# Performance work log

Measured on AMD Instinct MI355X. Metric: run time of the kernel, lower is better.

## Reference

```python
import jax, jax.numpy as jnp
import numpy as np

B, S, D = 2, 2048, 1024
H, HD = 16, 64


def setup_inputs() -> dict:
    key = jax.random.key(0)
    ks = jax.random.split(key, 10)
    scale = 1.0 / np.sqrt(D)
    inputs_q = jax.random.normal(ks[0], (B, S, D), dtype=jnp.float32)
    inputs_kv = jax.random.normal(ks[1], (B, S, D), dtype=jnp.float32)
    # causal mask, broadcast over batch: True = attend
    mask = jnp.broadcast_to(jnp.tril(jnp.ones((S, S), dtype=bool)), (B, S, S))
    Wq = jax.random.normal(ks[2], (D, H * HD), dtype=jnp.float32) * scale
    bq = jnp.zeros((H * HD,), dtype=jnp.float32)
    Wk = jax.random.normal(ks[3], (D, H * HD), dtype=jnp.float32) * scale
    bk = jnp.zeros((H * HD,), dtype=jnp.float32)
    Wv = jax.random.normal(ks[4], (D, H * HD), dtype=jnp.float32) * scale
    bv = jnp.zeros((H * HD,), dtype=jnp.float32)
    Wo = jax.random.normal(ks[5], (H * HD, D), dtype=jnp.float32) * scale
    bo = jnp.zeros((D,), dtype=jnp.float32)
    return {"inputs_q": inputs_q, "inputs_kv": inputs_kv, "mask": mask,
            "Wq": Wq, "bq": bq, "Wk": Wk, "bk": bk, "Wv": Wv, "bv": bv,
            "Wo": Wo, "bo": bo}


def reference(inputs_q, inputs_kv, mask, Wq, bq, Wk, bk, Wv, bv, Wo, bo):
    b, s_q, _ = inputs_q.shape
    s_k = inputs_kv.shape[1]
    # projections -> [B, S, H, HD]
    q = (inputs_q @ Wq + bq).reshape(b, s_q, H, HD)
    k = (inputs_kv @ Wk + bk).reshape(b, s_k, H, HD)
    v = (inputs_kv @ Wv + bv).reshape(b, s_k, H, HD)
    q = q / jnp.sqrt(jnp.asarray(HD, dtype=q.dtype))
    # scores: [B, H, Sq, Sk]
    attn = jnp.einsum('bqhd,bkhd->bhqk', q, k)
    m = mask[:, None, :, :]  # [B,1,Sq,Sk] broadcast over heads
    attn = jnp.where(m, attn, jnp.asarray(-1e30, dtype=attn.dtype))
    attn = jax.nn.softmax(attn, axis=-1)
    # dropout_rate = 0.0, deterministic -> identity
    out = jnp.einsum('bhqk,bkhd->bqhd', attn, v).reshape(b, s_q, H * HD)
    return out @ Wo + bo
```

## Files before the change

kernel.cpp:

```cpp
#include <hip/hip_runtime.h>

typedef __attribute__((ext_vector_type(4))) float f32x4;
typedef __attribute__((ext_vector_type(8))) short bf16x8;
typedef unsigned short u16;
typedef unsigned int u32;

#define AS1 __attribute__((address_space(1)))
#define AS3 __attribute__((address_space(3)))

__device__ __forceinline__ float fast_exp2(float x){
  return __builtin_amdgcn_exp2f(x);
}

__device__ __forceinline__ u16 f2bf(float x){
  u32 u = __float_as_uint(x);
  u += 0x7fffu + ((u >> 16) & 1u);
  return (u16)(u >> 16);
}
__device__ __forceinline__ u16 f2bf_fast(float x){
  return (u16)((__float_as_uint(x) + 0x8000u) >> 16);
}

__global__ __launch_bounds__(256) void cvt_qkv(const float* __restrict__ s0,
                                               const float* __restrict__ s1,
                                               u16* __restrict__ d0,
                                               u16* __restrict__ d1, int n4)
{
  int i = blockIdx.x * 256 + threadIdx.x;
  if (i >= n4) return;
  const float* src = blockIdx.y ? s1 : s0;
  u16* dst = blockIdx.y ? d1 : d0;
  float4 v = reinterpret_cast<const float4*>(src)[i];
  ushort4 o;
  o.x = f2bf(v.x); o.y = f2bf(v.y); o.z = f2bf(v.z); o.w = f2bf(v.w);
  reinterpret_cast<ushort4*>(dst)[i] = o;
}

__global__ __launch_bounds__(256) void transpose_cvt4(const float* __restrict__ W0,
                                                      const float* __restrict__ W1,
                                                      const float* __restrict__ W2,
                                                      const float* __restrict__ W3,
                                                      u16* __restrict__ dst)
{
  __shared__ float tile[32][33];
  const int z = blockIdx.z;
  const float* src = z == 0 ? W0 : z == 1 ? W1 : z == 2 ? W2 : W3;
  u16* d = dst + (size_t)z * 1024 * 1024;
  int tx = threadIdx.x & 31, ty = threadIdx.x >> 5;
  int k0 = blockIdx.x * 32, n0 = blockIdx.y * 32;
  for (int r = 0; r < 4; ++r)
    tile[ty + r * 8][tx] = src[(size_t)(k0 + ty + r * 8) * 1024 + n0 + tx];
  __syncthreads();
  for (int r = 0; r < 4; ++r)
    d[(size_t)(n0 + ty + r * 8) * 1024 + k0 + tx] = f2bf(tile[tx][ty + r * 8]);
}

__global__ __launch_bounds__(256) void gemm_qkv(const u16* __restrict__ Xq,
                                                const u16* __restrict__ Xkv,
                                                const u16* __restrict__ Wt,
                                                const float* __restrict__ bq,
                                                const float* __restrict__ bk,
                                                const float* __restrict__ bv,
                                                u16* __restrict__ Qb,
                                                u16* __restrict__ Kb,
                                                u16* __restrict__ Vt,
                                                int M, int K)
{
  __shared__ u16 lA[128 * 32];
  __shared__ u16 lB[128 * 32];
  const int tid = threadIdx.x;
  const int l = tid & 63, w = tid >> 6;
  const int wr = w >> 1, wc = w & 1;
  const int bm0 = blockIdx.x * 128, bn0 = blockIdx.y * 128;
  const int seg = bn0 >> 10;
  const int nloc0 = bn0 & 1023;
  const u16* A = seg ? Xkv : Xq;
  const float* bias = seg == 0 ? bq : seg == 1 ? bk : bv;
  const float scale = seg == 0 ? 0.125f * 1.44269504089f : 1.0f;
  const int lr = l & 15, lg = (l >> 4) * 8;

  f32x4 acc[4][4];
#pragma unroll
  for (int m = 0; m < 4; ++m)
#pragma unroll
    for (int n = 0; n < 4; ++n) acc[m][n] = (f32x4){0.f, 0.f, 0.f, 0.f};

  for (int k0 = 0; k0 < K; k0 += 32){
#pragma unroll
    for (int c = 0; c < 2; ++c){
      int e = (c * 256 + tid) * 8;
      int row = e >> 5, col = e & 31;
      __builtin_amdgcn_global_load_lds(
          (const AS1 u32*)(A + (size_t)(bm0 + row) * K + k0 + col),
          (AS3 u32*)(&lA[e]), 16, 0, 0);
      __builtin_amdgcn_global_load_lds(
          (const AS1 u32*)(Wt + (size_t)(bn0 + row) * K + k0 + col),
          (AS3 u32*)(&lB[e]), 16, 0, 0);
    }
    __syncthreads();
    bf16x8 aF[4], bF[4];
#pragma unroll
    for (int m = 0; m < 4; ++m)
      aF[m] = *reinterpret_cast<const bf16x8*>(&lA[(wr * 64 + m * 16 + lr) * 32 + lg]);
#pragma unroll
    for (int n = 0; n < 4; ++n)
      bF[n] = *reinterpret_cast<const bf16x8*>(&lB[(wc * 64 + n * 16 + lr) * 32 + lg]);
    __builtin_amdgcn_s_setprio(1);
#pragma unroll
    for (int m = 0; m < 4; ++m)
#pragma unroll
      for (int n = 0; n < 4; ++n)
        acc[m][n] = __builtin_amdgcn_mfma_f32_16x16x32_bf16(aF[m], bF[n], acc[m][n], 0, 0, 0);
    __builtin_amdgcn_s_setprio(0);
    __syncthreads();
  }

  const int r0 = (l >> 4) * 4;
  if (seg < 2){
    u16* C = seg == 0 ? Qb : Kb;
#pragma unroll
    for (int m = 0; m < 4; ++m)
#pragma unroll
      for (int n = 0; n < 4; ++n){
        int col = nloc0 + wc * 64 + n * 16 + lr;
        float bv_ = bias[col];
#pragma unroll
        for (int r = 0; r < 4; ++r){
          int row = bm0 + wr * 64 + m * 16 + r0 + r;
          C[(size_t)row * 1024 + col] = f2bf((acc[m][n][r] + bv_) * scale);
        }
      }
  } else {
#pragma unroll
    for (int m = 0; m < 4; ++m)
#pragma unroll
      for (int n = 0; n < 4; ++n){
        int col = nloc0 + wc * 64 + n * 16 + lr;
        float bv_ = bias[col];
        int h = col >> 6, hdl = col & 63;
#pragma unroll
        for (int r = 0; r < 4; ++r){
          int row = bm0 + wr * 64 + m * 16 + r0 + r;
          int b = row >> 11, kv = row & 2047;
          size_t off = ((size_t)(b * 16 + h)) * 131072 + (size_t)hdl * 2048 + kv;
          Vt[off] = f2bf(acc[m][n][r] + bv_);
        }
      }
  }
}

__global__ __launch_bounds__(256) void gemm_out(const u16* __restrict__ A,
                                                const u16* __restrict__ Bt,
                                                const float* __restrict__ bias,
                                                float* __restrict__ Cf,
                                                int M, int N, int K)
{
  __shared__ u16 lA[64 * 32];
  __shared__ u16 lB[128 * 32];
  const int tid = threadIdx.x;
  const int l = tid & 63, w = tid >> 6;
  const int wr = w >> 1, wc = w & 1;
  const int bm0 = blockIdx.x * 64, bn0 = blockIdx.y * 128;
  const int lr = l & 15, lg = (l >> 4) * 8;

  f32x4 acc[2][4];
#pragma unroll
  for (int m = 0; m < 2; ++m)
#pragma unroll
    for (int n = 0; n < 4; ++n) acc[m][n] = (f32x4){0.f, 0.f, 0.f, 0.f};

  for (int k0 = 0; k0 < K; k0 += 32){
    {
      int e = tid * 8;
      int row = e >> 5, col = e & 31;
      __builtin_amdgcn_global_load_lds(
          (const AS1 u32*)(A + (size_t)(bm0 + row) * K + k0 + col),
          (AS3 u32*)(&lA[e]), 16, 0, 0);
    }
#pragma unroll
    for (int c = 0; c < 2; ++c){
      int e = (c * 256 + tid) * 8;
      int row = e >> 5, col = e & 31;
      __builtin_amdgcn_global_load_lds(
          (const AS1 u32*)(Bt + (size_t)(bn0 + row) * K + k0 + col),
          (AS3 u32*)(&lB[e]), 16, 0, 0);
    }
    __syncthreads();
    bf16x8 aF[2], bF[4];
#pragma unroll
    for (int m = 0; m < 2; ++m)
      aF[m] = *reinterpret_cast<const bf16x8*>(&lA[(wr * 32 + m * 16 + lr) * 32 + lg]);
#pragma unroll
    for (int n = 0; n < 4; ++n)
      bF[n] = *reinterpret_cast<const bf16x8*>(&lB[(wc * 64 + n * 16 + lr) * 32 + lg]);
    __builtin_amdgcn_s_setprio(1);
#pragma unroll
    for (int m = 0; m < 2; ++m)
#pragma unroll
      for (int n = 0; n < 4; ++n)
        acc[m][n] = __builtin_amdgcn_mfma_f32_16x16x32_bf16(aF[m], bF[n], acc[m][n], 0, 0, 0);
    __builtin_amdgcn_s_setprio(0);
    __syncthreads();
  }

  const int r0 = (l >> 4) * 4;
#pragma unroll
  for (int m = 0; m < 2; ++m)
#pragma unroll
    for (int n = 0; n < 4; ++n){
      int col = bn0 + wc * 64 + n * 16 + lr;
      float bv_ = bias[col];
#pragma unroll
      for (int r = 0; r < 4; ++r){
        int row = bm0 + wr * 32 + m * 16 + r0 + r;
        Cf[(size_t)row * N + col] = acc[m][n][r] + bv_;
      }
    }
}


__global__ __launch_bounds__(512, 2) void attn_fwd(const u16* __restrict__ Qb,
                                                   const u16* __restrict__ Kb,
                                                   const u16* __restrict__ Vt,
                                                   u16* __restrict__ AO, int S)
{
  __shared__ u16 lK[64 * 64];
  __shared__ u16 lV[64 * 64];
  __shared__ u16 lP[8][16 * 72];
  const int tid = threadIdx.x, l = tid & 63, w = tid >> 6;
  const int j = blockIdx.x;
  const int xcd = j & 7;
  const int bh = xcd * 4 + ((j >> 3) & 3);
  const int p = j >> 5;
  const int bb = bh >> 4;
  const size_t baseQK = ((size_t)bb * S) * 1024 + (bh & 15) * 64;
  const u16* gK = Kb + baseQK;
  const u16* gV = Vt + (size_t)bh * 131072;
  const int lr = l & 15, g4 = l >> 4, lg = g4 * 8;

  u16* lPw = (u16*)lP[w];
  bf16x8 ones;
#pragma unroll
  for (int i = 0; i < 8; ++i) ones[i] = (short)0x3F80;

#define STAGE_KV(T) do{                                                       \
  int row_ = tid >> 3, ch_ = tid & 7, sc_ = (ch_ ^ (row_ & 7)) * 8;           \
  __builtin_amdgcn_global_load_lds(                                           \
      (const AS1 u32*)(gK + (size_t)(64 * (T) + row_) * 1024 + sc_),          \
      (AS3 u32*)(lK + tid * 8), 16, 0, 0);                                    \
  __builtin_amdgcn_global_load_lds(                                           \
      (const AS1 u32*)(gV + (size_t)row_ * 2048 + 64 * (T) + sc_),            \
      (AS3 u32*)(lV + tid * 8), 16, 0, 0);                                    \
}while(0)

#pragma unroll
  for (int pass = 0; pass < 2; ++pass){
    const int qt = pass ? (15 - p) : p;
    const int ntb = 2 * qt + 2;
    const int q0 = qt * 128 + w * 16;

    bf16x8 qf[2];
#pragma unroll
    for (int kc = 0; kc < 2; ++kc)
      qf[kc] = *reinterpret_cast<const bf16x8*>(
          Qb + baseQK + (size_t)(q0 + lr) * 1024 + kc * 32 + lg);

    f32x4 acc_o[4], acc_l;
    acc_l = (f32x4){0.f, 0.f, 0.f, 0.f};
#pragma unroll
    for (int n = 0; n < 4; ++n) acc_o[n] = (f32x4){0.f, 0.f, 0.f, 0.f};

    for (int t = 0; t < ntb; ++t){
      STAGE_KV(t);
      __syncthreads();

      if (64 * t <= q0 + 15){
        f32x4 sA[4];
#pragma unroll
        for (int np = 0; np < 4; ++np) sA[np] = (f32x4){0.f, 0.f, 0.f, 0.f};
        __builtin_amdgcn_s_setprio(1);
#pragma unroll
        for (int kc = 0; kc < 2; ++kc)
#pragma unroll
          for (int np = 0; np < 4; ++np){
            int row = np * 16 + lr, ch = kc * 4 + g4;
            bf16x8 kf = *reinterpret_cast<const bf16x8*>(
                reinterpret_cast<const char*>(lK) + row * 128 + ((ch ^ (row & 7)) << 4));
            sA[np] = __builtin_amdgcn_mfma_f32_16x16x32_bf16(qf[kc], kf, sA[np], 0, 0, 0);
          }
        __builtin_amdgcn_s_setprio(0);

        const bool needmask = (64 * t + 63 > q0);
        if (needmask){
#pragma unroll
          for (int np = 0; np < 4; ++np){
            int kvg = 64 * t + np * 16 + lr;
#pragma unroll
            for (int r = 0; r < 4; ++r){
              int qg = q0 + g4 * 4 + r;
              float e = fast_exp2(sA[np][r]);
              lPw[(g4 * 4 + r) * 72 + np * 16 + lr] = f2bf_fast((kvg <= qg) ? e : 0.f);
            }
          }
        } else {
#pragma unroll
          for (int np = 0; np < 4; ++np)
#pragma unroll
            for (int r = 0; r < 4; ++r)
              lPw[(g4 * 4 + r) * 72 + np * 16 + lr] = f2bf_fast(fast_exp2(sA[np][r]));
        }

        bf16x8 pf[2];
#pragma unroll
        for (int kc = 0; kc < 2; ++kc)
          pf[kc] = *reinterpret_cast<const bf16x8*>(
              reinterpret_cast<const char*>(lPw) + lr * 144 + (kc * 4 + g4) * 16);
        __builtin_amdgcn_s_setprio(1);
#pragma unroll
        for (int kc = 0; kc < 2; ++kc){
          acc_l = __builtin_amdgcn_mfma_f32_16x16x32_bf16(pf[kc], ones, acc_l, 0, 0, 0);
#pragma unroll
          for (int n = 0; n < 4; ++n){
            int row = n * 16 + lr, ch = kc * 4 + g4;
            bf16x8 vf = *reinterpret_cast<const bf16x8*>(
                reinterpret_cast<const char*>(lV) + row * 128 + ((ch ^ (row & 7)) << 4));
            acc_o[n] = __builtin_amdgcn_mfma_f32_16x16x32_bf16(pf[kc], vf, acc_o[n], 0, 0, 0);
          }
        }
        __builtin_amdgcn_s_setprio(0);
      }
      __syncthreads();
    }

    float inv[4];
#pragma unroll
    for (int r = 0; r < 4; ++r) inv[r] = 1.0f / acc_l[r];
#pragma unroll
    for (int n = 0; n < 4; ++n)
#pragma unroll
      for (int r = 0; r < 4; ++r){
        int row = q0 + g4 * 4 + r;
        AO[baseQK + (size_t)row * 1024 + n * 16 + lr] = f2bf(acc_o[n][r] * inv[r]);
      }
  }
#undef STAGE_KV
}

extern "C" void kernel_launch(void* const* d_in, const int* in_sizes, int n_in,
                              void* d_out, int out_size, void* d_ws, size_t ws_size,
                              hipStream_t stream)
{
  const float* inq  = (const float*)d_in[0];
  const float* inkv = (const float*)d_in[1];
  const float* Wq = (const float*)d_in[3];
  const float* bq = (const float*)d_in[4];
  const float* Wk = (const float*)d_in[5];
  const float* bk = (const float*)d_in[6];
  const float* Wv = (const float*)d_in[7];
  const float* bv = (const float*)d_in[8];
  const float* Wo = (const float*)d_in[9];
  const float* bo = (const float*)d_in[10];
  float* out = (float*)d_out;

  const int B = 2, S = 2048, D = 1024;
  const int M = B * S;

  char* ws = (char*)d_ws;
  const size_t MB = 1024ull * 1024ull;
  u16* Xq  = (u16*)(ws + 0 * MB);
  u16* Xkv = (u16*)(ws + 8 * MB);
  u16* Wt  = (u16*)(ws + 16 * MB);
  u16* Wot = (u16*)(ws + 22 * MB);
  u16* Qb  = (u16*)(ws + 24 * MB);
  u16* Kb  = (u16*)(ws + 32 * MB);
  u16* Vtg = (u16*)(ws + 40 * MB);
  u16* AOb = (u16*)(ws + 48 * MB);

  cvt_qkv<<<dim3(M * D / 4 / 256, 2), 256, 0, stream>>>(inq, inkv, Xq, Xkv, M * D / 4);

  transpose_cvt4<<<dim3(32, 32, 4), 256, 0, stream>>>(Wq, Wk, Wv, Wo, Wt);

  gemm_qkv<<<dim3(M / 128, 3072 / 128), 256, 0, stream>>>(Xq, Xkv, Wt, bq, bk, bv,
                                                          Qb, Kb, Vtg, M, D);

  attn_fwd<<<dim3(256), 512, 0, stream>>>(Qb, Kb, Vtg, AOb, S);

  gemm_out<<<dim3(M / 64, D / 128), 256, 0, stream>>>(AOb, Wot, bo, out, M, D, D);
}
```

Baseline: 134.0 us.

## Triple-buffer LDS in QKV GEMM with async prefetch two stages ahead

The QKV projection GEMM moves from a single LDS buffer to three, prefetching K-tiles two iterations ahead with global_load_lds, using explicit vmcnt waits and raw barriers. The goal is to overlap global-to-LDS loads with the MFMA work rather than stalling on each tile. In exchange LDS use per block triples, which could reduce occupancy. The loop is hardcoded to 32 iterations (K=1024), so it is tied to that K.

After: 123.3 us. -7.9%, faster.

```diff
diff --git a/kernel.cpp b/kernel.cpp
--- a/kernel.cpp
+++ b/kernel.cpp
@@ -7,6 +7,11 @@
 
 #define AS1 __attribute__((address_space(1)))
 #define AS3 __attribute__((address_space(3)))
+
+#define WAITVM(N) do{ asm volatile("s_waitcnt vmcnt(" #N ")" ::: "memory"); \
+                      __builtin_amdgcn_sched_barrier(0); }while(0)
+#define RAWBAR    do{ __builtin_amdgcn_s_barrier();                          \
+                      __builtin_amdgcn_sched_barrier(0); }while(0)
 
 __device__ __forceinline__ float fast_exp2(float x){
   return __builtin_amdgcn_exp2f(x);
@@ -66,8 +71,8 @@
                                                 u16* __restrict__ Vt,
                                                 int M, int K)
 {
-  __shared__ u16 lA[128 * 32];
-  __shared__ u16 lB[128 * 32];
+  __shared__ u16 lA[3][128 * 32];
+  __shared__ u16 lB[3][128 * 32];
   const int tid = threadIdx.x;
   const int l = tid & 63, w = tid >> 6;
   const int wr = w >> 1, wc = w & 1;
@@ -79,32 +84,43 @@
   const float scale = seg == 0 ? 0.125f * 1.44269504089f : 1.0f;
   const int lr = l & 15, lg = (l >> 4) * 8;
 
+#define STAGE_G(BI, KK) do{                                                   \
+  _Pragma("unroll") for (int c_ = 0; c_ < 2; ++c_){                           \
+    int e_ = (c_ * 256 + tid) * 8;                                            \
+    int row_ = e_ >> 5, col_ = e_ & 31;                                       \
+    __builtin_amdgcn_global_load_lds(                                         \
+        (const AS1 u32*)(A + (size_t)(bm0 + row_) * K + (KK) * 32 + col_),    \
+        (AS3 u32*)(&lA[BI][e_]), 16, 0, 0);                                   \
+    __builtin_amdgcn_global_load_lds(                                         \
+        (const AS1 u32*)(Wt + (size_t)(bn0 + row_) * K + (KK) * 32 + col_),   \
+        (AS3 u32*)(&lB[BI][e_]), 16, 0, 0);                                   \
+  }                                                                           \
+}while(0)
+
   f32x4 acc[4][4];
 #pragma unroll
   for (int m = 0; m < 4; ++m)
 #pragma unroll
     for (int n = 0; n < 4; ++n) acc[m][n] = (f32x4){0.f, 0.f, 0.f, 0.f};
 
-  for (int k0 = 0; k0 < K; k0 += 32){
-#pragma unroll
-    for (int c = 0; c < 2; ++c){
-      int e = (c * 256 + tid) * 8;
-      int row = e >> 5, col = e & 31;
-      __builtin_amdgcn_global_load_lds(
-          (const AS1 u32*)(A + (size_t)(bm0 + row) * K + k0 + col),
-          (AS3 u32*)(&lA[e]), 16, 0, 0);
-      __builtin_amdgcn_global_load_lds(
-          (const AS1 u32*)(Wt + (size_t)(bn0 + row) * K + k0 + col),
-          (AS3 u32*)(&lB[e]), 16, 0, 0);
-    }
-    __syncthreads();
+  STAGE_G(0, 0);
+  STAGE_G(1, 1);
+
+#pragma unroll
+  for (int k = 0; k < 32; ++k){
+    const int cur = k % 3;
+    if (k < 30){ STAGE_G((k + 2) % 3, k + 2); WAITVM(8); }
+    else if (k == 30){ WAITVM(4); }
+    else { WAITVM(0); }
+    RAWBAR;
+
     bf16x8 aF[4], bF[4];
 #pragma unroll
     for (int m = 0; m < 4; ++m)
-      aF[m] = *reinterpret_cast<const bf16x8*>(&lA[(wr * 64 + m * 16 + lr) * 32 + lg]);
+      aF[m] = *reinterpret_cast<const bf16x8*>(&lA[cur][(wr * 64 + m * 16 + lr) * 32 + lg]);
 #pragma unroll
     for (int n = 0; n < 4; ++n)
-      bF[n] = *reinterpret_cast<const bf16x8*>(&lB[(wc * 64 + n * 16 + lr) * 32 + lg]);
+      bF[n] = *reinterpret_cast<const bf16x8*>(&lB[cur][(wc * 64 + n * 16 + lr) * 32 + lg]);
     __builtin_amdgcn_s_setprio(1);
 #pragma unroll
     for (int m = 0; m < 4; ++m)
@@ -112,8 +128,9 @@
       for (int n = 0; n < 4; ++n)
         acc[m][n] = __builtin_amdgcn_mfma_f32_16x16x32_bf16(aF[m], bF[n], acc[m][n], 0, 0, 0);
     __builtin_amdgcn_s_setprio(0);
-    __syncthreads();
+    RAWBAR;
   }
+#undef STAGE_G
 
   const int r0 = (l >> 4) * 4;
   if (seg < 2){
@@ -217,7 +234,6 @@
       }
     }
 }
-
 
 __global__ __launch_bounds__(512, 2) void attn_fwd(const u16* __restrict__ Qb,
                                                    const u16* __restrict__ Kb,
```
